# Kernel tuning notes

Measured on AMD Instinct MI355X. Metric: run time of the kernel, lower is better.

## Reference

```python
import jax, jax.numpy as jnp
import numpy as np

B, Q, K, D, H = 2, 1024, 4096, 1024, 16
DH = D // H
LN_EPS = 1e-5


def setup_inputs() -> dict:
    key = jax.random.key(0)
    ks = jax.random.split(key, 10)
    queries = jax.random.normal(ks[0], (B, Q, D), jnp.float32)
    keys = jax.random.normal(ks[1], (B, K, D), jnp.float32)
    values = jax.random.normal(ks[2], (B, K, D), jnp.float32)
    # 128 words of 8 query tokens each: boundaries 0,8,...,1024 (sorted, unique)
    word_boundaries = jnp.arange(0, Q + 1, 8, dtype=jnp.int32)  # [129]
    # monotone map from query positions to char/key positions in [0, K]
    char_boundaries = jnp.sort(jax.random.randint(ks[3], (Q,), 0, K + 1, dtype=jnp.int32))
    s = 0.02
    ln_gamma = jnp.ones((D,), jnp.float32)
    ln_beta = jnp.zeros((D,), jnp.float32)
    in_proj_w = jax.random.normal(ks[4], (3 * D, D), jnp.float32) * s
    in_proj_b = jnp.zeros((3 * D,), jnp.float32)
    out_w = jax.random.normal(ks[5], (D, D), jnp.float32) * s
    out_b = jnp.zeros((D,), jnp.float32)
    return dict(queries=queries, keys=keys, values=values,
                word_boundaries=word_boundaries, char_boundaries=char_boundaries,
                ln_gamma=ln_gamma, ln_beta=ln_beta,
                in_proj_w=in_proj_w, in_proj_b=in_proj_b,
                out_w=out_w, out_b=out_b)


def char_aware_mask(wb, cb, q_len, k_len):
    """Vectorized version of the per-word python loop.
    Float mask of 0/1 (PyTorch ADDS a float attn_mask to the scores)."""
    ws, we = wb[:-1], wb[1:]                     # word start/end in query coords [nW]
    nW = ws.shape[0]
    cs = cb[ws]                                  # char span start per word
    ce = cb[we - 1]                              # char span end per word
    q = jnp.arange(q_len)
    i = jnp.clip(jnp.searchsorted(wb, q, side='right') - 1, 0, nW - 1)  # word id per query row
    valid = (q >= ws[i]) & (q < we[i])           # rows actually written by the loop
    j = jnp.arange(k_len)[None, :]               # [1, K]
    in_char = (j >= cs[i][:, None]) & (j < ce[i][:, None])
    # prev word: keys [wb[i-1], wb[i]) (query-coord indices used on key axis, as in source)
    ps = ws[jnp.maximum(i - 1, 0)]
    in_prev = (i > 0)[:, None] & (j >= ps[:, None]) & (j < ws[i][:, None])
    # next word: keys [wb[i+1], wb[i+2])
    ns = we[i]
    ne = wb[jnp.minimum(i + 2, nW)]
    in_next = (i < nW - 1)[:, None] & (j >= ns[:, None]) & (j < ne[:, None])
    return (valid[:, None] & (in_char | in_prev | in_next)).astype(jnp.float32)


def reference(queries, keys, values, word_boundaries, char_boundaries,
              ln_gamma, ln_beta, in_proj_w, in_proj_b, out_w, out_b):
    b, q_len, d = queries.shape
    k_len = keys.shape[1]
    mask = char_aware_mask(word_boundaries, char_boundaries, q_len, k_len)  # [Q, K]
    # LayerNorm(queries)
    mu = jnp.mean(queries, axis=-1, keepdims=True)
    var = jnp.var(queries, axis=-1, keepdims=True)
    x = (queries - mu) * jax.lax.rsqrt(var + LN_EPS) * ln_gamma + ln_beta
    # MultiheadAttention(x, keys, values, attn_mask=mask) -- float mask added to logits
    wq, wk, wv = jnp.split(in_proj_w, 3, axis=0)
    bq, bk, bv = jnp.split(in_proj_b, 3)
    qh = (x @ wq.T + bq).reshape(b, q_len, H, DH)
    kh = (keys @ wk.T + bk).reshape(b, k_len, H, DH)
    vh = (values @ wv.T + bv).reshape(b, k_len, H, DH)
    scale = 1.0 / jnp.sqrt(jnp.asarray(DH, queries.dtype))
    scores = jnp.einsum('bqhd,bkhd->bhqk', qh * scale, kh) + mask[None, None]
    attn = jax.nn.softmax(scores, axis=-1)
    ctx = jnp.einsum('bhqk,bkhd->bqhd', attn, vh).reshape(b, q_len, d)
    out = ctx @ out_w.T + out_b
    # residual; dropout is identity at inference
    return queries + out
```

## Files before the change

### kernel.cpp

```cpp
#include <hip/hip_runtime.h>
#include <hip/hip_bf16.h>


typedef __attribute__((ext_vector_type(8))) short bf16x8;
typedef __attribute__((ext_vector_type(4))) float f32x4;
typedef __attribute__((ext_vector_type(16))) float f32x16;

#define L2E 1.44269504088896341f
#define CSCALE (0.125f * L2E)
#define NSPLIT 4

__device__ __forceinline__ short f2bf(float f) {
  __hip_bfloat16 h = __float2bfloat16(f);
  return reinterpret_cast<short&>(h);
}

__device__ __forceinline__ unsigned cvtpk(float a, float b) {
  unsigned r;
  asm("v_cvt_pk_bf16_f32 %0, %1, %2" : "=v"(r) : "v"(a), "v"(b));
  return r;
}

__device__ __forceinline__ float fexp2(float x) {
#if __has_builtin(__builtin_amdgcn_exp2f)
  return __builtin_amdgcn_exp2f(x);
#else
  float r;
  asm("v_exp_f32 %0, %1" : "=v"(r) : "v"(x));
  return r;
#endif
}

__device__ __forceinline__ void halfswap(unsigned a, unsigned b, unsigned& x, unsigned& y) {
#if __has_builtin(__builtin_amdgcn_permlane32_swap)
  auto r = __builtin_amdgcn_permlane32_swap(a, b, false, false);
  x = (unsigned)r[0];
  y = (unsigned)r[1];
#else
  unsigned ca = (unsigned)__shfl_xor((int)a, 32);
  unsigned cb = (unsigned)__shfl_xor((int)b, 32);
  bool h = ((threadIdx.x & 63) >> 5) != 0;
  x = h ? cb : a;
  y = h ? b : ca;
#endif
}

__device__ __forceinline__ void gload16(const void* g, void* l) {
  __builtin_amdgcn_global_load_lds(
      (const __attribute__((address_space(1))) void*)g,
      (__attribute__((address_space(3))) void*)l, 16, 0, 0);
}

template <int N>
__device__ __forceinline__ void phase_end() {
  __builtin_amdgcn_sched_barrier(0);
  if constexpr (N == 8)
    asm volatile("s_waitcnt vmcnt(8)" ::: "memory");
  else if constexpr (N == 6)
    asm volatile("s_waitcnt vmcnt(6)" ::: "memory");
  else if constexpr (N == 4)
    asm volatile("s_waitcnt vmcnt(4)" ::: "memory");
  else if constexpr (N == 2)
    asm volatile("s_waitcnt vmcnt(2)" ::: "memory");
  else
    asm volatile("s_waitcnt vmcnt(0)" ::: "memory");
  __builtin_amdgcn_s_barrier();
  __builtin_amdgcn_sched_barrier(0);
}

__device__ __forceinline__ void wait_lgkm0() {
  __builtin_amdgcn_sched_barrier(0);
  asm volatile("s_waitcnt lgkmcnt(0)" ::: "memory");
  __builtin_amdgcn_sched_barrier(0);
}

__global__ __launch_bounds__(256) void prep_kernel(const float* __restrict__ w,
                                                   const float* __restrict__ o,
                                                   short* __restrict__ dw,
                                                   short* __restrict__ dof,
                                                   const float* __restrict__ x,
                                                   const float* __restrict__ gamma,
                                                   const float* __restrict__ beta,
                                                   short* __restrict__ xout,
                                                   const int* __restrict__ wb,
                                                   const int* __restrict__ cb,
                                                   int* __restrict__ iv,
                                                   const float* __restrict__ keys,
                                                   const float* __restrict__ values,
                                                   short* __restrict__ kbf,
                                                   short* __restrict__ vbf) {
  const int blk = blockIdx.x;
  const int t = threadIdx.x;
  if (blk < 4096) {
    long i = ((long)blk * 256 + t) * 4;
    const float* s;
    short* d;
    if (i < 3145728) { s = w + i; d = dw + i; }
    else { s = o + (i - 3145728); d = dof + (i - 3145728); }
    float4 xv = *(const float4*)s;
    uint2 r;
    r.x = cvtpk(xv.x, xv.y);
    r.y = cvtpk(xv.z, xv.w);
    *(uint2*)d = r;
  } else if (blk < 6144) {
    const int row = blk - 4096;
    float4 v = ((const float4*)(x + (size_t)row * 1024))[t];
    float s = v.x + v.y + v.z + v.w;
    float ss = v.x * v.x + v.y * v.y + v.z * v.z + v.w * v.w;
#pragma unroll
    for (int d = 32; d; d >>= 1) { s += __shfl_xor(s, d); ss += __shfl_xor(ss, d); }
    __shared__ float red[8];
    int wv2 = t >> 6, lane = t & 63;
    if (lane == 0) { red[wv2] = s; red[4 + wv2] = ss; }
    __syncthreads();
    s = red[0] + red[1] + red[2] + red[3];
    ss = red[4] + red[5] + red[6] + red[7];
    float mean = s * (1.0f / 1024.0f);
    float var = ss * (1.0f / 1024.0f) - mean * mean;
    float rstd = rsqrtf(var + 1e-5f);
    float4 g = ((const float4*)gamma)[t];
    float4 b = ((const float4*)beta)[t];
    uint2 oo;
    oo.x = cvtpk((v.x - mean) * rstd * g.x + b.x, (v.y - mean) * rstd * g.y + b.y);
    oo.y = cvtpk((v.z - mean) * rstd * g.z + b.z, (v.w - mean) * rstd * g.w + b.w);
    ((uint2*)(xout + (size_t)row * 1024))[t] = oo;
  } else if (blk < 6148) {
    int q = (blk - 6144) * 256 + t;
    if (q >= 1024) return;
    int cnt = 0;
    for (int k = 0; k < 129; ++k) cnt += (wb[k] <= q) ? 1 : 0;
    int i = cnt - 1;
    i = i < 0 ? 0 : (i > 127 ? 127 : i);
    bool valid = (q >= wb[i]) && (q < wb[i + 1]);
    int cs = 0, ce = 0, pl = 0, ph = 0, nl = 0, nh = 0;
    if (valid) {
      cs = cb[wb[i]];
      ce = cb[wb[i + 1] - 1];
      if (i > 0) { pl = wb[i - 1]; ph = wb[i]; }
      if (i < 127) { nl = wb[i + 1]; nh = wb[(i + 2 <= 128) ? i + 2 : 128]; }
    }
    int* p = iv + q * 8;
    p[0] = cs; p[1] = ce; p[2] = pl; p[3] = ph; p[4] = nl; p[5] = nh; p[6] = 0; p[7] = 0;
  } else {
    long i = ((long)(blk - 6148) * 256 + t) * 4;
    const float* s;
    short* d;
    if (i < 8388608) { s = keys + i; d = kbf + i; }
    else { s = values + (i - 8388608); d = vbf + (i - 8388608); }
    float4 xv = *(const float4*)s;
    uint2 r;
    r.x = cvtpk(xv.x, xv.y);
    r.y = cvtpk(xv.z, xv.w);
    *(uint2*)d = r;
  }
}

__device__ __forceinline__ unsigned inrange3(int key, const int* p) {
  bool m = (key >= p[0] && key < p[1]) || (key >= p[2] && key < p[3]) ||
           (key >= p[4] && key < p[5]);
  return m ? 1u : 0u;
}

__global__ __launch_bounds__(256) void mask_frag_kernel(const int* __restrict__ iv,
                                                        uint4* __restrict__ pmf) {
  int idx = blockIdx.x * 256 + threadIdx.x;
  int lane = idx & 63;
  int wg = (idx >> 6) & 31;
  int t = idx >> 11;
  int l31 = lane & 31, hi = lane >> 5;
  uint4 o = {0u, 0u, 0u, 0u};
  if (!hi) {
    int key0 = t * 64 + l31, key1 = key0 + 32;
    const int* p0 = iv + (wg * 32 + 0) * 8;
    const int* p1 = iv + (wg * 32 + 8) * 8;
    const int* p2 = iv + (wg * 32 + 16) * 8;
    const int* p3 = iv + (wg * 32 + 24) * 8;
    unsigned b0 = inrange3(key0, p0), b1 = inrange3(key0, p1);
    unsigned b2 = inrange3(key0, p2), b3 = inrange3(key0, p3);
    o.x = (b0 | (b1 << 16)) * 0x3F80u;
    o.y = (b2 | (b3 << 16)) * 0x3F80u;
    b0 = inrange3(key1, p0); b1 = inrange3(key1, p1);
    b2 = inrange3(key1, p2); b3 = inrange3(key1, p3);
    o.z = (b0 | (b1 << 16)) * 0x3F80u;
    o.w = (b2 | (b3 << 16)) * 0x3F80u;
  }
  pmf[idx] = o;
}

__device__ __forceinline__ void kv256_body(short* lds, const short* __restrict__ Agl,
                                           const short* __restrict__ Bgl,
                                           const float* __restrict__ bias,
                                           short* __restrict__ Cout, int mode,
                                           int bx, int by) {
  const int tid = (int)threadIdx.x;
  const int lane = tid & 63;
  const int w = tid >> 6;
  const int wm = w >> 2, wn = w & 3;
  const int l16 = lane & 15, lhi = lane >> 4;
  const int gc8 = (lane & 7) ^ (lane >> 3);
  const int lr = lane >> 3;
  const int rsw = (l16 & 7) << 4;
  const int m0 = bx * 256, n0 = by * 256;

  f32x4 acc[8][4];
#pragma unroll
  for (int i = 0; i < 8; ++i)
#pragma unroll
    for (int j = 0; j < 4; ++j) acc[i][j] = f32x4{0.f, 0.f, 0.f, 0.f};

  auto SU = [&](int k, int unit) {
    const int k0 = k * 64;
    short* base = lds + (k & 1) * 32768;
#pragma unroll
    for (int j = 0; j < 2; ++j) {
      int i = w * 2 + j;
      int ch;
      bool isA;
      if (unit == 1)      { ch = (i < 8) ? i : i + 8;       isA = true; }
      else if (unit == 4) { ch = 8 + ((i < 8) ? i : i + 8); isA = true; }
      else if (unit == 2) { ch = (i >> 2) * 8 + (i & 3);    isA = false; }
      else                { ch = 4 + (i >> 2) * 8 + (i & 3); isA = false; }
      const short* g = isA ? (Agl + (size_t)(m0 + ch * 8 + lr) * 1024 + k0 + gc8 * 8)
                           : (Bgl + (size_t)(n0 + ch * 8 + lr) * 1024 + k0 + gc8 * 8);
      gload16(g, base + (isA ? 0 : 16384) + ch * 512);
    }
  };

  bf16x8 af[4][2], b0[2][2], b1[2][2];
  auto LDA = [&](int bsel, int qm) {
    const char* cA = (const char*)(lds + bsel * 32768);
#pragma unroll
    for (int mt = 0; mt < 4; ++mt)
#pragma unroll
      for (int kk = 0; kk < 2; ++kk) {
        int row = wm * 128 + qm * 64 + mt * 16 + l16;
        af[mt][kk] = *(const bf16x8*)(cA + row * 128 + ((kk * 64 + lhi * 16) ^ rsw));
      }
  };
  auto LDB = [&](int bsel, int qn, bf16x8 (&bf)[2][2]) {
    const char* cB = (const char*)(lds + bsel * 32768) + 32768;
#pragma unroll
    for (int nt = 0; nt < 2; ++nt)
#pragma unroll
      for (int kk = 0; kk < 2; ++kk) {
        int row = wn * 64 + qn * 32 + nt * 16 + l16;
        bf[nt][kk] = *(const bf16x8*)(cB + row * 128 + ((kk * 64 + lhi * 16) ^ rsw));
      }
  };
  auto MM = [&](int qm, int qn, bf16x8 (&bf)[2][2]) {
    __builtin_amdgcn_s_setprio(1);
#pragma unroll
    for (int kk = 0; kk < 2; ++kk)
#pragma unroll
      for (int mt = 0; mt < 4; ++mt)
#pragma unroll
        for (int nt = 0; nt < 2; ++nt)
          acc[qm * 4 + mt][qn * 2 + nt] = __builtin_amdgcn_mfma_f32_16x16x32_bf16(
              af[mt][kk], bf[nt][kk], acc[qm * 4 + mt][qn * 2 + nt], 0, 0, 0);
    __builtin_amdgcn_s_setprio(0);
  };

  SU(0, 1); SU(0, 2); SU(0, 3); SU(0, 4);
  SU(1, 1); SU(1, 2);
  phase_end<8>();

#pragma unroll 2
  for (int k = 0; k < 14; ++k) {
    const int bs = k & 1;
    LDA(bs, 0); LDB(bs, 0, b0); SU(k + 1, 3);
    wait_lgkm0(); MM(0, 0, b0); phase_end<8>();
    LDB(bs, 1, b1); SU(k + 1, 4);
    wait_lgkm0(); MM(0, 1, b1); phase_end<8>();
    LDA(bs, 1); SU(k + 2, 1);
    wait_lgkm0(); MM(1, 0, b0); phase_end<8>();
    SU(k + 2, 2);
    MM(1, 1, b1); phase_end<8>();
  }
  {
    LDA(0, 0); LDB(0, 0, b0); SU(15, 3);
    wait_lgkm0(); MM(0, 0, b0); phase_end<8>();
    LDB(0, 1, b1); SU(15, 4);
    wait_lgkm0(); MM(0, 1, b1); phase_end<8>();
    LDA(0, 1);
    wait_lgkm0(); MM(1, 0, b0); phase_end<8>();
    MM(1, 1, b1); phase_end<4>();
  }
  {
    LDA(1, 0); LDB(1, 0, b0);
    wait_lgkm0(); MM(0, 0, b0); phase_end<2>();
    LDB(1, 1, b1);
    wait_lgkm0(); MM(0, 1, b1); phase_end<0>();
    LDA(1, 1);
    wait_lgkm0(); MM(1, 0, b0);
    MM(1, 1, b1);
  }

#pragma unroll
  for (int mt = 0; mt < 8; ++mt)
#pragma unroll
    for (int nt = 0; nt < 4; ++nt) {
      int n = n0 + wn * 64 + nt * 16 + l16;
#pragma unroll
      for (int r = 0; r < 4; ++r) {
        int m = m0 + wm * 128 + mt * 16 + lhi * 4 + r;
        float v = acc[mt][nt][r];
        if (mode == 0) {
          int bb = m >> 12, key = m & 4095;
          int hh = n >> 6, dhl = n & 63;
          Cout[((size_t)((bb * 16 + hh) * 4096 + key)) * 64 + dhl] = f2bf(v + bias[n]);
        } else {
          int bb = n >> 12, key = n & 4095;
          Cout[((size_t)(bb * 1024 + m)) * 4096 + key] = f2bf(v + bias[m]);
        }
      }
    }
}

__device__ __forceinline__ void gemmQO_body(short* lA, short* lB,
                                            const short* __restrict__ A,
                                            const short* __restrict__ W,
                                            const float* __restrict__ bias,
                                            const float* __restrict__ resid,
                                            void* __restrict__ Cout, int mode,
                                            float scale, int bxi, int byi) {
  const int lane = threadIdx.x & 63;
  const int w = threadIdx.x >> 6;
  const int m0 = bxi * 64;
  const int n0 = byi * 128;
  const int wm = w >> 2, wn = w & 3;
  const int l16 = lane & 15, lhi = lane >> 4;

  const int gc8 = (lane & 7) ^ (lane >> 3);
  const int lr = lane >> 3;
  const int rsw = (l16 & 7) << 4;

  f32x4 zero = {0.f, 0.f, 0.f, 0.f};
  f32x4 acc[2][2];
#pragma unroll
  for (int i = 0; i < 2; ++i)
#pragma unroll
    for (int j = 0; j < 2; ++j) acc[i][j] = zero;

  for (int k0 = 0; k0 < 1024; k0 += 64) {
    __syncthreads();
#pragma unroll
    for (int j = 0; j < 3; ++j) {
      int c = w * 3 + j;
      if (c < 8)
        gload16(A + (size_t)(m0 + c * 8 + lr) * 1024 + k0 + gc8 * 8, &lA[c * 512]);
      else
        gload16(W + (size_t)(n0 + (c - 8) * 8 + lr) * 1024 + k0 + gc8 * 8,
                &lB[(c - 8) * 512]);
    }
    __syncthreads();
    bf16x8 af[2][2], bfr[2][2];
#pragma unroll
    for (int mt = 0; mt < 2; ++mt)
#pragma unroll
      for (int kk = 0; kk < 2; ++kk)
        af[mt][kk] = *(const bf16x8*)((const char*)lA + (wm * 32 + mt * 16 + l16) * 128 +
                                      ((kk * 64 + lhi * 16) ^ rsw));
#pragma unroll
    for (int nt = 0; nt < 2; ++nt)
#pragma unroll
      for (int kk = 0; kk < 2; ++kk)
        bfr[nt][kk] = *(const bf16x8*)((const char*)lB + (wn * 32 + nt * 16 + l16) * 128 +
                                       ((kk * 64 + lhi * 16) ^ rsw));
#pragma unroll
    for (int kk = 0; kk < 2; ++kk)
#pragma unroll
      for (int mt = 0; mt < 2; ++mt)
#pragma unroll
        for (int nt = 0; nt < 2; ++nt)
          acc[mt][nt] = __builtin_amdgcn_mfma_f32_16x16x32_bf16(af[mt][kk], bfr[nt][kk],
                                                                acc[mt][nt], 0, 0, 0);
  }

#pragma unroll
  for (int mt = 0; mt < 2; ++mt)
#pragma unroll
    for (int nt = 0; nt < 2; ++nt) {
      int col = n0 + wn * 32 + nt * 16 + l16;
      float bs = bias[col];
#pragma unroll
      for (int r = 0; r < 4; ++r) {
        int row = m0 + wm * 32 + mt * 16 + lhi * 4 + r;
        float v = acc[mt][nt][r] + bs;
        if (mode == 0) {
          ((short*)Cout)[(size_t)row * 1024 + col] = f2bf(v * scale);
        } else {
          size_t idx = (size_t)row * 1024 + col;
          ((float*)Cout)[idx] = v + resid[idx];
        }
      }
    }
}

__global__ __launch_bounds__(512, 2) void megaGemm_kernel(const short* __restrict__ kbf,
                                                          const short* __restrict__ wk,
                                                          const float* __restrict__ kbias,
                                                          const short* __restrict__ wv,
                                                          const short* __restrict__ vbf,
                                                          const float* __restrict__ vbias,
                                                          short* __restrict__ khp,
                                                          short* __restrict__ vhT,
                                                          const short* __restrict__ xb,
                                                          const short* __restrict__ wq,
                                                          const float* __restrict__ qbias,
                                                          short* __restrict__ qhb) {
  __shared__ __attribute__((aligned(16))) short lds[65536];
  int id = blockIdx.x;
  if (id < 128) {
    kv256_body(lds, kbf, wk, kbias, khp, 0, id & 31, id >> 5);
  } else if (id < 256) {
    int i2 = id & 127;
    kv256_body(lds, wv, vbf, vbias, vhT, 1, i2 >> 5, i2 & 31);
  } else {
    int i2 = id - 256;
    gemmQO_body(lds, lds + 4096, xb, wq, qbias, nullptr, qhb, 0, CSCALE, i2 & 31, i2 >> 5);
  }
}

__global__ __launch_bounds__(512, 4) void gemmQO_kernel(const short* __restrict__ A,
                                                        const short* __restrict__ W,
                                                        const float* __restrict__ bias,
                                                        const float* __restrict__ resid,
                                                        void* __restrict__ Cout, int mode,
                                                        float scale) {
  __shared__ __attribute__((aligned(16))) short lA[4096];
  __shared__ __attribute__((aligned(16))) short lB[8192];
  gemmQO_body(lA, lB, A, W, bias, resid, Cout, mode, scale, blockIdx.x, blockIdx.y);
}

__global__ __launch_bounds__(256) void attn9_kernel(const short* __restrict__ qh,
                                                    const short* __restrict__ khp,
                                                    const short* __restrict__ vtp,
                                                    const uint4* __restrict__ pmf,
                                                    short* __restrict__ pacc,
                                                    float* __restrict__ pml) {
  const int tid = threadIdx.x;
  const int lane = tid & 63;
  const int w = tid >> 6;
  const int l31 = lane & 31;
  const int hi = lane >> 5;
  const int id = blockIdx.x;
  const int qb = id >> 7;
  const int g = id & 127;
  const int bh = g >> 2;
  const int ks = g & 3;
  const int b = bh >> 4, h = bh & 15;

  __shared__ __attribute__((aligned(16))) short sK[2][4096];
  __shared__ __attribute__((aligned(16))) short sV[2][4096];

  const int wq0 = qb * 128 + w * 32;
  const int qrow = wq0 + l31;
  bf16x8 qf0, qf1, qf2, qf3;
  {
    const short* qp = qh + ((size_t)(b * 1024 + qrow)) * 1024 + h * 64 + hi * 8;
    qf0 = *(const bf16x8*)(qp);
    qf1 = *(const bf16x8*)(qp + 16);
    qf2 = *(const bf16x8*)(qp + 32);
    qf3 = *(const bf16x8*)(qp + 48);
  }

  bf16x8 bmv;
  {
    union { unsigned u[4]; bf16x8 v; } t;
    t.u[0] = t.u[1] = t.u[2] = t.u[3] = 0;
    int lj = l31 >> 3;
    unsigned val = 0x3FB9u << (16 * (lj & 1));
    if (!hi) t.u[lj >> 1] = val;
    bmv = t.v;
  }

  bf16x8 bones;
  {
    union { unsigned u[4]; bf16x8 v; } t;
    t.u[0] = t.u[1] = t.u[2] = t.u[3] = 0x3F803F80u;
    bones = t.v;
  }

  f32x16 fzero;
#pragma unroll
  for (int i = 0; i < 16; ++i) fzero[i] = 0.f;

  const int kchunk = ks * 1024;
  const int sub = (lane & 7) ^ (lane >> 3);
  const int r8 = lane >> 3;
  const size_t kbase_g = ((size_t)bh * 4096 + kchunk) * 64;
  const size_t vbase_g = ((size_t)bh * 64) * 4096 + (size_t)kchunk;
  const uint4* pmfp = pmf + ((size_t)(ks * 16) * 32 + qb * 4 + w) * 64 + lane;

  f32x16 acc0, acc1, acc2;
#pragma unroll
  for (int i = 0; i < 16; ++i) { acc0[i] = 0.f; acc1[i] = 0.f; acc2[i] = 0.f; }

  const int koff_swz = (lane & 7) << 4;

  auto STAGE = [&](int buf, int t) {
    int kt = t * 64;
#pragma unroll
    for (int q2 = 0; q2 < 2; ++q2) {
      int ch = w * 2 + q2;
      gload16(khp + kbase_g + (size_t)(kt + ch * 8 + r8) * 64 + sub * 8,
              (short*)sK[buf] + ch * 512);
      gload16(vtp + vbase_g + (size_t)(ch * 8 + r8) * 4096 + kt + sub * 8,
              (short*)sV[buf] + ch * 512);
    }
  };

  uint4 mf_cur = pmfp[0];
  uint4 mf_next = mf_cur;
  STAGE(0, 0);
  __syncthreads();
  int buf = 0;

  for (int t = 0; t < 16; ++t) {
    if (t < 15) {
      STAGE(buf ^ 1, t + 1);
      mf_next = pmfp[(size_t)(t + 1) * 2048];
    }

    bf16x8 am0, am1;
    {
      union { unsigned u[4]; bf16x8 v; } f;
      f.u[0] = mf_cur.x; f.u[1] = mf_cur.y; f.u[2] = 0; f.u[3] = 0;
      am0 = f.v;
      f.u[0] = mf_cur.z; f.u[1] = mf_cur.w;
      am1 = f.v;
    }

    __builtin_amdgcn_s_setprio(1);
    f32x16 ss0 = __builtin_amdgcn_mfma_f32_32x32x16_bf16(am0, bmv, fzero, 0, 0, 0);
    f32x16 ss1 = __builtin_amdgcn_mfma_f32_32x32x16_bf16(am1, bmv, fzero, 0, 0, 0);
#pragma unroll
    for (int c = 0; c < 4; ++c) {
      int off = (c * 32 + hi * 16) ^ koff_swz;
      bf16x8 k0 = *(const bf16x8*)((const char*)sK[buf] + l31 * 128 + off);
      bf16x8 k1 = *(const bf16x8*)((const char*)sK[buf] + (32 + l31) * 128 + off);
      bf16x8 qc = (c == 0) ? qf0 : (c == 1) ? qf1 : (c == 2) ? qf2 : qf3;
      ss0 = __builtin_amdgcn_mfma_f32_32x32x16_bf16(k0, qc, ss0, 0, 0, 0);
      ss1 = __builtin_amdgcn_mfma_f32_32x32x16_bf16(k1, qc, ss1, 0, 0, 0);
    }
    __builtin_amdgcn_s_setprio(0);

#pragma unroll
    for (int r = 0; r < 16; ++r) {
      ss0[r] = fexp2(ss0[r]);
      ss1[r] = fexp2(ss1[r]);
    }

    bf16x8 pa0, pa1, pa2, pa3;
    {
      unsigned a01 = cvtpk(ss0[0], ss0[1]), a23 = cvtpk(ss0[2], ss0[3]);
      unsigned a45 = cvtpk(ss0[4], ss0[5]), a67 = cvtpk(ss0[6], ss0[7]);
      unsigned a89 = cvtpk(ss0[8], ss0[9]), aAB = cvtpk(ss0[10], ss0[11]);
      unsigned aCD = cvtpk(ss0[12], ss0[13]), aEF = cvtpk(ss0[14], ss0[15]);
      union { unsigned u[4]; bf16x8 v; } f;
      halfswap(a01, a45, f.u[0], f.u[2]);
      halfswap(a23, a67, f.u[1], f.u[3]);
      pa0 = f.v;
      halfswap(a89, aCD, f.u[0], f.u[2]);
      halfswap(aAB, aEF, f.u[1], f.u[3]);
      pa1 = f.v;
    }
    {
      unsigned a01 = cvtpk(ss1[0], ss1[1]), a23 = cvtpk(ss1[2], ss1[3]);
      unsigned a45 = cvtpk(ss1[4], ss1[5]), a67 = cvtpk(ss1[6], ss1[7]);
      unsigned a89 = cvtpk(ss1[8], ss1[9]), aAB = cvtpk(ss1[10], ss1[11]);
      unsigned aCD = cvtpk(ss1[12], ss1[13]), aEF = cvtpk(ss1[14], ss1[15]);
      union { unsigned u[4]; bf16x8 v; } f;
      halfswap(a01, a45, f.u[0], f.u[2]);
      halfswap(a23, a67, f.u[1], f.u[3]);
      pa2 = f.v;
      halfswap(a89, aCD, f.u[0], f.u[2]);
      halfswap(aAB, aEF, f.u[1], f.u[3]);
      pa3 = f.v;
    }

    __builtin_amdgcn_s_setprio(1);
#pragma unroll
    for (int kb16 = 0; kb16 < 4; ++kb16) {
      int off = (kb16 * 32 + hi * 16) ^ koff_swz;
      bf16x8 v0 = *(const bf16x8*)((const char*)sV[buf] + l31 * 128 + off);
      bf16x8 v1 = *(const bf16x8*)((const char*)sV[buf] + (32 + l31) * 128 + off);
      bf16x8 pa = (kb16 == 0) ? pa0 : (kb16 == 1) ? pa1 : (kb16 == 2) ? pa2 : pa3;
      acc0 = __builtin_amdgcn_mfma_f32_32x32x16_bf16(pa, v0, acc0, 0, 0, 0);
      acc1 = __builtin_amdgcn_mfma_f32_32x32x16_bf16(pa, v1, acc1, 0, 0, 0);
      acc2 = __builtin_amdgcn_mfma_f32_32x32x16_bf16(pa, bones, acc2, 0, 0, 0);
    }
    __builtin_amdgcn_s_setprio(0);
    __syncthreads();
    buf ^= 1;
    mf_cur = mf_next;
  }

  short* paccp = pacc + (((size_t)ks * 32 + bh) * 1024) * 64;
#pragma unroll
  for (int r = 0; r < 16; r += 2) {
    int q0 = wq0 + ((r & 3) + 8 * (r >> 2)) + 4 * hi;
    int q1 = wq0 + (((r + 1) & 3) + 8 * ((r + 1) >> 2)) + 4 * hi;
    unsigned u0 = cvtpk(acc0[r], acc0[r + 1]);
    unsigned u1 = cvtpk(acc1[r], acc1[r + 1]);
    paccp[(size_t)q0 * 64 + l31] = (short)(u0 & 0xffffu);
    paccp[(size_t)q1 * 64 + l31] = (short)(u0 >> 16);
    paccp[(size_t)q0 * 64 + 32 + l31] = (short)(u1 & 0xffffu);
    paccp[(size_t)q1 * 64 + 32 + l31] = (short)(u1 >> 16);
  }
  if (l31 == 0) {
    float* mlp = pml + ((size_t)ks * 32 + bh) * 1024;
#pragma unroll
    for (int r = 0; r < 16; ++r) {
      int q = wq0 + ((r & 3) + 8 * (r >> 2)) + 4 * hi;
      mlp[q] = acc2[r];
    }
  }
}

__global__ __launch_bounds__(256) void combine_kernel(const short* __restrict__ pacc,
                                                      const float* __restrict__ pml,
                                                      short* __restrict__ ctx) {
  int idx = blockIdx.x * 256 + threadIdx.x;
  int dh4 = idx & 15;
  int row = idx >> 4;
  int bh = row >> 10, q = row & 1023;
  float L = 0.f, o0 = 0.f, o1 = 0.f, o2 = 0.f, o3 = 0.f;
#pragma unroll
  for (int k = 0; k < NSPLIT; ++k) {
    L += pml[((size_t)k * 32 + bh) * 1024 + q];
    uint2 u = *(const uint2*)&pacc[(((size_t)k * 32 + bh) * 1024 + q) * 64 + dh4 * 4];
    unsigned a = u.x, b2 = u.y;
    unsigned t0 = a << 16, t1 = a & 0xffff0000u, t2 = b2 << 16, t3 = b2 & 0xffff0000u;
    o0 += reinterpret_cast<float&>(t0);
    o1 += reinterpret_cast<float&>(t1);
    o2 += reinterpret_cast<float&>(t2);
    o3 += reinterpret_cast<float&>(t3);
  }
  float inv = 1.0f / L;
  uint2 st;
  st.x = cvtpk(o0 * inv, o1 * inv);
  st.y = cvtpk(o2 * inv, o3 * inv);
  int b = bh >> 4, h = bh & 15;
  *(uint2*)&ctx[((size_t)(b * 1024 + q)) * 1024 + h * 64 + dh4 * 4] = st;
}

extern "C" void kernel_launch(void* const* d_in, const int* in_sizes, int n_in,
                              void* d_out, int out_size, void* d_ws, size_t ws_size,
                              hipStream_t stream) {
  const float* queries = (const float*)d_in[0];
  const float* keys    = (const float*)d_in[1];
  const float* values  = (const float*)d_in[2];
  const int*   wb      = (const int*)d_in[3];
  const int*   cb      = (const int*)d_in[4];
  const float* gamma   = (const float*)d_in[5];
  const float* beta    = (const float*)d_in[6];
  const float* ipw     = (const float*)d_in[7];
  const float* ipb     = (const float*)d_in[8];
  const float* ow      = (const float*)d_in[9];
  const float* ob      = (const float*)d_in[10];
  float* out = (float*)d_out;

  char* p = (char*)d_ws;
  short* xb  = (short*)p; p += (size_t)2048 * 1024 * 2;
  short* kb  = (short*)p; p += (size_t)8192 * 1024 * 2;
  short* vb  = (short*)p; p += (size_t)8192 * 1024 * 2;
  short* wpb = (short*)p; p += (size_t)3072 * 1024 * 2;
  short* owb = (short*)p; p += (size_t)1024 * 1024 * 2;
  short* qhb = (short*)p; p += (size_t)2048 * 1024 * 2;
  short* khp = (short*)p; p += (size_t)8192 * 1024 * 2;
  short* vhT = (short*)p; p += (size_t)8192 * 1024 * 2;
  short* ctx = (short*)p; p += (size_t)2048 * 1024 * 2;
  int* iv = (int*)p; p += (size_t)1024 * 8 * 4;
  uint4* pmf = (uint4*)p; p += (size_t)64 * 32 * 64 * 16;
  if ((size_t)(p - (char*)d_ws) > ws_size) return;

  short* pacc = kb;
  float* pml  = (float*)wpb;

  prep_kernel<<<22532, 256, 0, stream>>>(ipw, ow, wpb, owb, queries, gamma, beta, xb,
                                         wb, cb, iv, keys, values, kb, vb);
  mask_frag_kernel<<<512, 256, 0, stream>>>(iv, pmf);

  megaGemm_kernel<<<512, 512, 0, stream>>>(kb, wpb + 1048576, ipb + 1024,
                                           wpb + 2097152, vb, ipb + 2048,
                                           khp, vhT, xb, wpb, ipb, qhb);

  attn9_kernel<<<1024, 256, 0, stream>>>(qhb, khp, vhT, pmf, pacc, pml);
  combine_kernel<<<2048, 256, 0, stream>>>(pacc, pml, ctx);

  gemmQO_kernel<<<dim3(32, 8), 512, 0, stream>>>(ctx, owb, ob, queries, out, 2, 1.f);
}
```

Baseline: 154.2 us.

## Restructure attention K/V pipeline to prefetch two tiles ahead with explicit vmcnt waits

```diff
diff --git a/kernel.cpp b/kernel.cpp
--- a/kernel.cpp
+++ b/kernel.cpp
@@ -58,6 +58,8 @@
     asm volatile("s_waitcnt vmcnt(8)" ::: "memory");
   else if constexpr (N == 6)
     asm volatile("s_waitcnt vmcnt(6)" ::: "memory");
+  else if constexpr (N == 5)
+    asm volatile("s_waitcnt vmcnt(5)" ::: "memory");
   else if constexpr (N == 4)
     asm volatile("s_waitcnt vmcnt(4)" ::: "memory");
   else if constexpr (N == 2)
@@ -71,6 +73,12 @@
 __device__ __forceinline__ void wait_lgkm0() {
   __builtin_amdgcn_sched_barrier(0);
   asm volatile("s_waitcnt lgkmcnt(0)" ::: "memory");
+  __builtin_amdgcn_sched_barrier(0);
+}
+
+__device__ __forceinline__ void lds_barrier() {
+  __builtin_amdgcn_sched_barrier(0);
+  __builtin_amdgcn_s_barrier();
   __builtin_amdgcn_sched_barrier(0);
 }
 
@@ -432,12 +440,12 @@
   gemmQO_body(lA, lB, A, W, bias, resid, Cout, mode, scale, blockIdx.x, blockIdx.y);
 }
 
-__global__ __launch_bounds__(256) void attn9_kernel(const short* __restrict__ qh,
-                                                    const short* __restrict__ khp,
-                                                    const short* __restrict__ vtp,
-                                                    const uint4* __restrict__ pmf,
-                                                    short* __restrict__ pacc,
-                                                    float* __restrict__ pml) {
+__global__ __launch_bounds__(256) void attn10_kernel(const short* __restrict__ qh,
+                                                     const short* __restrict__ khp,
+                                                     const short* __restrict__ vtp,
+                                                     const uint4* __restrict__ pmf,
+                                                     short* __restrict__ pacc,
+                                                     float* __restrict__ pml) {
   const int tid = threadIdx.x;
   const int lane = tid & 63;
   const int w = tid >> 6;
@@ -510,24 +518,13 @@
     }
   };
 
-  uint4 mf_cur = pmfp[0];
-  uint4 mf_next = mf_cur;
-  STAGE(0, 0);
-  __syncthreads();
-  int buf = 0;
-
-  for (int t = 0; t < 16; ++t) {
-    if (t < 15) {
-      STAGE(buf ^ 1, t + 1);
-      mf_next = pmfp[(size_t)(t + 1) * 2048];
-    }
-
+  auto TILE = [&](int buf, uint4 mf) {
     bf16x8 am0, am1;
     {
       union { unsigned u[4]; bf16x8 v; } f;
-      f.u[0] = mf_cur.x; f.u[1] = mf_cur.y; f.u[2] = 0; f.u[3] = 0;
+      f.u[0] = mf.x; f.u[1] = mf.y; f.u[2] = 0; f.u[3] = 0;
       am0 = f.v;
-      f.u[0] = mf_cur.z; f.u[1] = mf_cur.w;
+      f.u[0] = mf.z; f.u[1] = mf.w;
       am1 = f.v;
     }
 
@@ -591,10 +588,32 @@
       acc2 = __builtin_amdgcn_mfma_f32_32x32x16_bf16(pa, bones, acc2, 0, 0, 0);
     }
     __builtin_amdgcn_s_setprio(0);
-    __syncthreads();
-    buf ^= 1;
+  };
+
+  __builtin_amdgcn_sched_barrier(0);
+  uint4 mf_cur = pmfp[0];
+  __builtin_amdgcn_sched_barrier(0);
+  STAGE(0, 0);
+  __builtin_amdgcn_sched_barrier(0);
+  uint4 mf_next = pmfp[2048];
+  __builtin_amdgcn_sched_barrier(0);
+  STAGE(1, 1);
+  phase_end<5>();
+
+  for (int t = 0; t < 14; ++t) {
+    int buf = t & 1;
+    TILE(buf, mf_cur);
+    lds_barrier();
+    uint4 mf_n2 = pmfp[(size_t)(t + 2) * 2048];
+    __builtin_amdgcn_sched_barrier(0);
+    STAGE(buf, t + 2);
+    phase_end<5>();
     mf_cur = mf_next;
-  }
+    mf_next = mf_n2;
+  }
+  TILE(0, mf_cur);
+  phase_end<0>();
+  TILE(1, mf_next);
 
   short* paccp = pacc + (((size_t)ks * 32 + bh) * 1024) * 64;
 #pragma unroll
@@ -686,7 +705,7 @@
                                            wpb + 2097152, vb, ipb + 2048,
                                            khp, vhT, xb, wpb, ipb, qhb);
 
-  attn9_kernel<<<1024, 256, 0, stream>>>(qhb, khp, vhT, pmf, pacc, pml);
+  attn10_kernel<<<1024, 256, 0, stream>>>(qhb, khp, vhT, pmf, pacc, pml);
   combine_kernel<<<2048, 256, 0, stream>>>(pacc, pml, ctx);
 
   gemmQO_kernel<<<dim3(32, 8), 512, 0, stream>>>(ctx, owb, ob, queries, out, 2, 1.f);
```

Result: no change. 155.2 us (+0.6%).
